# Optimization experiments

Hardware: AMD Instinct MI355X
Metric: run time of the kernel (lower is better)

Reference implementation:

```python
import jax, jax.numpy as jnp
import numpy as np

BN_EPS = 1e-5


def _preconv(x, bn_gamma, bn_beta, bn_mean, bn_var, conv_w, conv_b):
    # nn.Sequential(ReLU, BatchNorm2d(eval mode), Conv2d(in->32, k=1))
    x = jax.nn.relu(x)
    scale = bn_gamma * jax.lax.rsqrt(bn_var + BN_EPS)          # [C]
    x = x * scale[None, :, None, None] + (bn_beta - bn_mean * scale)[None, :, None, None]
    # 1x1 conv == channel matmul
    x = jnp.einsum('bchw,oc->bohw', x, conv_w) + conv_b[None, :, None, None]
    return x


def setup_inputs() -> dict:
    key = jax.random.key(0)
    ks = jax.random.split(key, 8)
    B, Cin, H, W = 8, 80, 160, 320
    return {
        'features_L': jax.random.normal(ks[0], (B, Cin, H, W), dtype=jnp.float32),
        'features_R': jax.random.normal(ks[1], (B, Cin, H, W), dtype=jnp.float32),
        'bn_gamma': jax.random.uniform(ks[2], (Cin,), dtype=jnp.float32, minval=0.5, maxval=1.5),
        'bn_beta': jax.random.normal(ks[3], (Cin,), dtype=jnp.float32) * 0.1,
        'bn_mean': jax.random.normal(ks[4], (Cin,), dtype=jnp.float32) * 0.1,
        'bn_var': jax.random.uniform(ks[5], (Cin,), dtype=jnp.float32, minval=0.5, maxval=1.5),
        'conv_w': jax.random.normal(ks[6], (32, Cin), dtype=jnp.float32) * 0.05,
        'conv_b': jax.random.normal(ks[7], (32,), dtype=jnp.float32) * 0.05,
    }


def reference(features_L, features_R, bn_gamma, bn_beta, bn_mean, bn_var, conv_w, conv_b):
    VOLUME_SIZE = 48  # init kwarg; num_groups = 1 (hardcoded)
    featL = _preconv(features_L, bn_gamma, bn_beta, bn_mean, bn_var, conv_w, conv_b)
    featR = _preconv(features_R, bn_gamma, bn_beta, bn_mean, bn_var, conv_w, conv_b)
    B, C, H, W = featL.shape
    planes = []
    for i in range(VOLUME_SIZE):
        # shift featR right by i with zero padding; zeros in cols < i match the
        # zero-initialized volume entries of the original loop.
        if i > 0:
            shifted = jnp.pad(featR, ((0, 0), (0, 0), (0, 0), (i, 0)))[:, :, :, :W]
        else:
            shifted = featR
        planes.append(jnp.mean(featL * shifted, axis=1))  # [B,H,W]
    volume = jnp.stack(planes, axis=1)  # [B, D, H, W]
    return volume
```

## Files before the change

kernel.cpp:

```cpp
#include <hip/hip_runtime.h>

#define WW   320
#define HH   160
#define CIN  80
#define COUT 32
#define DD   48
#define NB   8
#define VP   84

typedef __bf16 bf16x8 __attribute__((ext_vector_type(8)));
typedef __bf16 bf16x4 __attribute__((ext_vector_type(4)));
typedef float  float4v __attribute__((ext_vector_type(4)));

__global__ __launch_bounds__(320, 2)
void vol_kernel(const float* __restrict__ inL, const float* __restrict__ inR,
                const float* __restrict__ gamma, const float* __restrict__ beta,
                const float* __restrict__ bnmean, const float* __restrict__ bnvar,
                const float* __restrict__ convw, const float* __restrict__ convb,
                float* __restrict__ out)
{
    __shared__ __align__(16) __bf16 fLs[WW * COUT];
    __shared__ __align__(16) __bf16 fRs[WW * COUT];
    __shared__ __align__(16) char   uni[WW * COUT * 2];
    __shared__ __align__(16) float  scs[96];
    __shared__ float  shs[80];
    __shared__ float  biasp[32];
    __shared__ float  scratch[320];

    __bf16* xs2 = (__bf16*)uni;
    float*  vol = (float*)uni;

    const int t = threadIdx.x;
    const int b = blockIdx.x / HH;
    const int h = blockIdx.x % HH;
    const size_t HW = (size_t)HH * WW;
    const int wave = t >> 6, lane = t & 63, ln15 = lane & 15, quad = lane >> 4;
    const int w = t;
    const int sw = (w >> 1) & 3;

    if (t < CIN) {
        float sc = gamma[t] * rsqrtf(bnvar[t] + 1e-5f);
        scs[t] = sc;
        shs[t] = fmaf(-bnmean[t], sc, beta[t]);
    } else if (t < 96) {
        scs[t] = 0.f;
    }
    __syncthreads();

    bf16x8 afr[2][3];
    #pragma unroll
    for (int mt = 0; mt < 2; ++mt) {
        #pragma unroll
        for (int kk = 0; kk < 3; ++kk) {
            const int c0 = kk * 32 + quad * 8;
            bf16x8 a;
            if (c0 < CIN) {
                const float* wp = convw + (mt * 16 + ln15) * CIN + c0;
                float4v w0 = *(const float4v*)wp;
                float4v w1 = *(const float4v*)(wp + 4);
                float4v s0 = *(const float4v*)(scs + c0);
                float4v s1 = *(const float4v*)(scs + c0 + 4);
                #pragma unroll
                for (int j = 0; j < 4; ++j) {
                    a[j]     = (__bf16)(w0[j] * s0[j]);
                    a[j + 4] = (__bf16)(w1[j] * s1[j]);
                }
            } else {
                #pragma unroll
                for (int j = 0; j < 8; ++j) a[j] = (__bf16)0.f;
            }
            afr[mt][kk] = a;
        }
    }
    {
        const int o = t & 31, part = t >> 5;
        float p = 0.f;
        #pragma unroll
        for (int j = 0; j < 8; ++j) {
            int c = part * 8 + j;
            p = fmaf(shs[c], convw[o * CIN + c], p);
        }
        scratch[part * 32 + o] = p;
    }
    __syncthreads();
    if (t < 32) {
        float s = convb[t];
        #pragma unroll
        for (int pt = 0; pt < 10; ++pt) s += scratch[pt * 32 + t];
        biasp[t] = s;
    }

    #pragma unroll 1
    for (int img = 0; img < 2; ++img) {
        const float* __restrict__ px =
            (img ? inR : inL) + ((size_t)b * CIN * HH + h) * WW + w;
        __bf16* f = img ? fRs : fLs;

        float4v acc[2][4];
        #pragma unroll
        for (int mt = 0; mt < 2; ++mt)
            #pragma unroll
            for (int nn = 0; nn < 4; ++nn) acc[mt][nn] = (float4v){0.f, 0.f, 0.f, 0.f};

        float y[32];
        #pragma unroll
        for (int u = 0; u < 32; ++u) y[u] = px[(size_t)u * HW];
        #pragma unroll
        for (int g = 0; g < 4; ++g) {
            bf16x8 pk;
            #pragma unroll
            for (int j = 0; j < 8; ++j) pk[j] = (__bf16)fmaxf(y[g * 8 + j], 0.f);
            *(bf16x8*)(xs2 + w * 32 + ((g ^ sw) << 3)) = pk;
        }
        __syncthreads();

        #pragma unroll
        for (int kk = 0; kk < 3; ++kk) {
            if (kk < 2) {
                #pragma unroll
                for (int u = 0; u < 32; ++u) {
                    int c = (kk + 1) * 32 + u;
                    y[u] = (c < CIN) ? px[(size_t)c * HW] : 0.f;
                }
            }
            #pragma unroll
            for (int nn = 0; nn < 4; ++nn) {
                const int wr = (nn * 5 + wave) * 16 + ln15;
                bf16x8 bv = *(const bf16x8*)(xs2 + wr * 32 +
                                             ((quad ^ ((wr >> 1) & 3)) << 3));
                acc[0][nn] = __builtin_amdgcn_mfma_f32_16x16x32_bf16(afr[0][kk], bv, acc[0][nn], 0, 0, 0);
                acc[1][nn] = __builtin_amdgcn_mfma_f32_16x16x32_bf16(afr[1][kk], bv, acc[1][nn], 0, 0, 0);
            }
            __syncthreads();
            if (kk < 2) {
                #pragma unroll
                for (int g = 0; g < 4; ++g) {
                    bf16x8 pk;
                    #pragma unroll
                    for (int j = 0; j < 8; ++j) pk[j] = (__bf16)fmaxf(y[g * 8 + j], 0.f);
                    *(bf16x8*)(xs2 + w * 32 + ((g ^ sw) << 3)) = pk;
                }
                __syncthreads();
            }
        }

        #pragma unroll
        for (int nn = 0; nn < 4; ++nn) {
            const int wg  = (nn * 5 + wave) * 16 + ln15;
            const int swg = (wg >> 1) & 3;
            #pragma unroll
            for (int mt = 0; mt < 2; ++mt) {
                float4v bi = *(const float4v*)(biasp + mt * 16 + quad * 4);
                bf16x4 o4;
                #pragma unroll
                for (int r = 0; r < 4; ++r)
                    o4[r] = (__bf16)(acc[mt][nn][r] + bi[r]);
                const int g = 2 * mt + (quad >> 1);
                *(bf16x4*)(f + wg * 32 + ((g ^ swg) << 3) + (quad & 1) * 4) = o4;
            }
        }
    }
    __syncthreads();

    for (int pass = 0; pass < 4; ++pass) {
        for (int k = wave; k < 20; k += 5) {
            const int two = k >> 2;
            const int d   = k & 3;
            const int tw  = pass * 5 + two;
            const int tj  = tw - d;
            if (tj >= 0) {
                const int wr = tw * 16 + ln15;
                const int jr = tj * 16 + ln15;
                bf16x8 av = *(const bf16x8*)(fLs + wr * 32 +
                                             ((quad ^ ((wr >> 1) & 3)) << 3));
                bf16x8 bv = *(const bf16x8*)(fRs + jr * 32 +
                                             ((quad ^ ((jr >> 1) & 3)) << 3));
                float4v cz = {0.f, 0.f, 0.f, 0.f};
                float4v dv = __builtin_amdgcn_mfma_f32_16x16x32_bf16(av, bv, cz, 0, 0, 0);
                #pragma unroll
                for (int r = 0; r < 4; ++r) {
                    int row = quad * 4 + r;
                    int i = 16 * d + row - ln15;
                    if (i >= 0 && i < DD)
                        vol[i * VP + two * 16 + row] = dv[r] * (1.f / 32.f);
                }
            }
        }
        __syncthreads();

        for (int s = t; s < DD * 20; s += 320) {
            int i = s / 20, q = s - i * 20;
            int wg0 = pass * 80 + q * 4;
            float4v v = *(const float4v*)(vol + i * VP + q * 4);
            #pragma unroll
            for (int e = 0; e < 4; ++e)
                if (wg0 + e < i) v[e] = 0.f;
            *(float4v*)(out + ((size_t)(b * DD + i) * HH + h) * WW + wg0) = v;
        }
        __syncthreads();
    }
}

extern "C" void kernel_launch(void* const* d_in, const int* in_sizes, int n_in,
                              void* d_out, int out_size, void* d_ws, size_t ws_size,
                              hipStream_t stream) {
    const float* inL    = (const float*)d_in[0];
    const float* inR    = (const float*)d_in[1];
    const float* gamma  = (const float*)d_in[2];
    const float* beta   = (const float*)d_in[3];
    const float* bnmean = (const float*)d_in[4];
    const float* bnvar  = (const float*)d_in[5];
    const float* convw  = (const float*)d_in[6];
    const float* convb  = (const float*)d_in[7];
    float* out = (float*)d_out;

    dim3 grid(NB * HH);
    dim3 block(320);
    vol_kernel<<<grid, block, 0, stream>>>(inL, inR, gamma, beta, bnmean, bnvar,
                                           convw, convb, out);
}
```

Before: 335.2 us.

## Feed conv MFMA directly from registers, shrink LDS, raise occupancy

```diff
diff --git a/kernel.cpp b/kernel.cpp
--- a/kernel.cpp
+++ b/kernel.cpp
@@ -6,13 +6,12 @@
 #define COUT 32
 #define DD   48
 #define NB   8
-#define VP   84
+#define VP2  68
 
 typedef __bf16 bf16x8 __attribute__((ext_vector_type(8)));
-typedef __bf16 bf16x4 __attribute__((ext_vector_type(4)));
 typedef float  float4v __attribute__((ext_vector_type(4)));
 
-__global__ __launch_bounds__(320, 2)
+__global__ __launch_bounds__(320, 4)
 void vol_kernel(const float* __restrict__ inL, const float* __restrict__ inR,
                 const float* __restrict__ gamma, const float* __restrict__ beta,
                 const float* __restrict__ bnmean, const float* __restrict__ bnvar,
@@ -21,22 +20,19 @@
 {
     __shared__ __align__(16) __bf16 fLs[WW * COUT];
     __shared__ __align__(16) __bf16 fRs[WW * COUT];
-    __shared__ __align__(16) char   uni[WW * COUT * 2];
-    __shared__ __align__(16) float  scs[96];
-    __shared__ float  shs[80];
-    __shared__ float  biasp[32];
-    __shared__ float  scratch[320];
-
-    __bf16* xs2 = (__bf16*)uni;
-    float*  vol = (float*)uni;
+    __shared__ __align__(16) float  vol[DD * VP2];
+    __shared__ float biasp[32];
+
+    float* scs     = (float*)fLs;
+    float* shs     = scs + 96;
+    float* scratch = shs + 80;
 
     const int t = threadIdx.x;
     const int b = blockIdx.x / HH;
     const int h = blockIdx.x % HH;
     const size_t HW = (size_t)HH * WW;
     const int wave = t >> 6, lane = t & 63, ln15 = lane & 15, quad = lane >> 4;
-    const int w = t;
-    const int sw = (w >> 1) & 3;
+    const int wb = wave * 64;
 
     if (t < CIN) {
         float sc = gamma[t] * rsqrtf(bnvar[t] + 1e-5f);
@@ -47,15 +43,15 @@
     }
     __syncthreads();
 
-    bf16x8 afr[2][3];
+    bf16x8 bfr[2][3];
     #pragma unroll
-    for (int mt = 0; mt < 2; ++mt) {
+    for (int ot = 0; ot < 2; ++ot) {
         #pragma unroll
         for (int kk = 0; kk < 3; ++kk) {
             const int c0 = kk * 32 + quad * 8;
             bf16x8 a;
             if (c0 < CIN) {
-                const float* wp = convw + (mt * 16 + ln15) * CIN + c0;
+                const float* wp = convw + (ot * 16 + ln15) * CIN + c0;
                 float4v w0 = *(const float4v*)wp;
                 float4v w1 = *(const float4v*)(wp + 4);
                 float4v s0 = *(const float4v*)(scs + c0);
@@ -69,7 +65,7 @@
                 #pragma unroll
                 for (int j = 0; j < 8; ++j) a[j] = (__bf16)0.f;
             }
-            afr[mt][kk] = a;
+            bfr[ot][kk] = a;
         }
     }
     {
@@ -89,84 +85,77 @@
         for (int pt = 0; pt < 10; ++pt) s += scratch[pt * 32 + t];
         biasp[t] = s;
     }
+    __syncthreads();
 
     #pragma unroll 1
     for (int img = 0; img < 2; ++img) {
-        const float* __restrict__ px =
-            (img ? inR : inL) + ((size_t)b * CIN * HH + h) * WW + w;
+        const float* __restrict__ pbase =
+            (img ? inR : inL) + ((size_t)b * CIN * HH + h) * WW;
         __bf16* f = img ? fRs : fLs;
 
-        float4v acc[2][4];
-        #pragma unroll
-        for (int mt = 0; mt < 2; ++mt)
+        const float bi0 = biasp[ln15];
+        const float bi1 = biasp[16 + ln15];
+        float4v acc[4][2];
+        #pragma unroll
+        for (int nt = 0; nt < 4; ++nt) {
+            acc[nt][0] = (float4v){bi0, bi0, bi0, bi0};
+            acc[nt][1] = (float4v){bi1, bi1, bi1, bi1};
+        }
+
+        float y[3][8];
+        auto LOADF = [&](int ft, float (&yy)[8]) {
+            const int nt = ft / 3, kk = ft - nt * 3;
+            if (kk == 2 && quad >= 2) {
+                #pragma unroll
+                for (int j = 0; j < 8; ++j) yy[j] = 0.f;
+            } else {
+                const float* pp = pbase + (size_t)(kk * 32 + quad * 8) * HW
+                                        + (wb + nt * 16 + ln15);
+                #pragma unroll
+                for (int j = 0; j < 8; ++j) yy[j] = pp[(size_t)j * HW];
+            }
+        };
+
+        LOADF(0, y[0]);
+        LOADF(1, y[1]);
+        #pragma unroll
+        for (int ft = 0; ft < 12; ++ft) {
+            if (ft < 10) LOADF(ft + 2, y[(ft + 2) % 3]);
+            const int nt = ft / 3, kk = ft - nt * 3;
+            bf16x8 a;
+            {
+                float (&yy)[8] = y[ft % 3];
+                #pragma unroll
+                for (int j = 0; j < 8; ++j) a[j] = (__bf16)fmaxf(yy[j], 0.f);
+            }
+            acc[nt][0] = __builtin_amdgcn_mfma_f32_16x16x32_bf16(a, bfr[0][kk], acc[nt][0], 0, 0, 0);
+            acc[nt][1] = __builtin_amdgcn_mfma_f32_16x16x32_bf16(a, bfr[1][kk], acc[nt][1], 0, 0, 0);
+        }
+
+        #pragma unroll
+        for (int nt = 0; nt < 4; ++nt) {
+            const int wr0 = wb + nt * 16 + quad * 4;
             #pragma unroll
-            for (int nn = 0; nn < 4; ++nn) acc[mt][nn] = (float4v){0.f, 0.f, 0.f, 0.f};
-
-        float y[32];
-        #pragma unroll
-        for (int u = 0; u < 32; ++u) y[u] = px[(size_t)u * HW];
-        #pragma unroll
-        for (int g = 0; g < 4; ++g) {
-            bf16x8 pk;
-            #pragma unroll
-            for (int j = 0; j < 8; ++j) pk[j] = (__bf16)fmaxf(y[g * 8 + j], 0.f);
-            *(bf16x8*)(xs2 + w * 32 + ((g ^ sw) << 3)) = pk;
-        }
-        __syncthreads();
-
-        #pragma unroll
-        for (int kk = 0; kk < 3; ++kk) {
-            if (kk < 2) {
-                #pragma unroll
-                for (int u = 0; u < 32; ++u) {
-                    int c = (kk + 1) * 32 + u;
-                    y[u] = (c < CIN) ? px[(size_t)c * HW] : 0.f;
+            for (int r = 0; r < 4; ++r) {
+                const int w  = wr0 + r;
+                const int sw = (w >> 1) & 3;
+                #pragma unroll
+                for (int ot = 0; ot < 2; ++ot) {
+                    const int o = ot * 16 + ln15;
+                    f[w * 32 + ((((o >> 3) ^ sw)) << 3) + (o & 7)] =
+                        (__bf16)acc[nt][ot][r];
                 }
             }
-            #pragma unroll
-            for (int nn = 0; nn < 4; ++nn) {
-                const int wr = (nn * 5 + wave) * 16 + ln15;
-                bf16x8 bv = *(const bf16x8*)(xs2 + wr * 32 +
-                                             ((quad ^ ((wr >> 1) & 3)) << 3));
-                acc[0][nn] = __builtin_amdgcn_mfma_f32_16x16x32_bf16(afr[0][kk], bv, acc[0][nn], 0, 0, 0);
-                acc[1][nn] = __builtin_amdgcn_mfma_f32_16x16x32_bf16(afr[1][kk], bv, acc[1][nn], 0, 0, 0);
-            }
-            __syncthreads();
-            if (kk < 2) {
-                #pragma unroll
-                for (int g = 0; g < 4; ++g) {
-                    bf16x8 pk;
-                    #pragma unroll
-                    for (int j = 0; j < 8; ++j) pk[j] = (__bf16)fmaxf(y[g * 8 + j], 0.f);
-                    *(bf16x8*)(xs2 + w * 32 + ((g ^ sw) << 3)) = pk;
-                }
-                __syncthreads();
-            }
-        }
-
-        #pragma unroll
-        for (int nn = 0; nn < 4; ++nn) {
-            const int wg  = (nn * 5 + wave) * 16 + ln15;
-            const int swg = (wg >> 1) & 3;
-            #pragma unroll
-            for (int mt = 0; mt < 2; ++mt) {
-                float4v bi = *(const float4v*)(biasp + mt * 16 + quad * 4);
-                bf16x4 o4;
-                #pragma unroll
-                for (int r = 0; r < 4; ++r)
-                    o4[r] = (__bf16)(acc[mt][nn][r] + bi[r]);
-                const int g = 2 * mt + (quad >> 1);
-                *(bf16x4*)(f + wg * 32 + ((g ^ swg) << 3) + (quad & 1) * 4) = o4;
-            }
-        }
-    }
-    __syncthreads();
-
-    for (int pass = 0; pass < 4; ++pass) {
-        for (int k = wave; k < 20; k += 5) {
+        }
+    }
+    __syncthreads();
+
+    #pragma unroll 1
+    for (int pass = 0; pass < 5; ++pass) {
+        for (int k = wave; k < 16; k += 5) {
             const int two = k >> 2;
             const int d   = k & 3;
-            const int tw  = pass * 5 + two;
+            const int tw  = pass * 4 + two;
             const int tj  = tw - d;
             if (tj >= 0) {
                 const int wr = tw * 16 + ln15;
@@ -182,20 +171,20 @@
                     int row = quad * 4 + r;
                     int i = 16 * d + row - ln15;
                     if (i >= 0 && i < DD)
-                        vol[i * VP + two * 16 + row] = dv[r] * (1.f / 32.f);
+                        vol[i * VP2 + two * 16 + row] = dv[r] * (1.f / 32.f);
                 }
             }
         }
         __syncthreads();
 
-        for (int s = t; s < DD * 20; s += 320) {
-            int i = s / 20, q = s - i * 20;
-            int wg0 = pass * 80 + q * 4;
-            float4v v = *(const float4v*)(vol + i * VP + q * 4);
+        for (int s = t; s < DD * 16; s += 320) {
+            int i = s >> 4, q = s & 15;
+            int w0 = pass * 64 + q * 4;
+            float4v v = *(const float4v*)(vol + i * VP2 + q * 4);
             #pragma unroll
             for (int e = 0; e < 4; ++e)
-                if (wg0 + e < i) v[e] = 0.f;
-            *(float4v*)(out + ((size_t)(b * DD + i) * HH + h) * WW + wg0) = v;
+                if (w0 + e < i) v[e] = 0.f;
+            *(float4v*)(out + ((size_t)(b * DD + i) * HH + h) * WW + w0) = v;
         }
         __syncthreads();
     }
```

Measured after the change: 352.5 us. 5.1% more time.

## Split fused kernel into preconv and volume kernels via bf16 workspace

Applied to the files above, without the earlier changes.

```diff
diff --git a/kernel.cpp b/kernel.cpp
--- a/kernel.cpp
+++ b/kernel.cpp
@@ -7,10 +7,229 @@
 #define DD   48
 #define NB   8
 #define VP   84
+#define VP2  68
 
 typedef __bf16 bf16x8 __attribute__((ext_vector_type(8)));
 typedef __bf16 bf16x4 __attribute__((ext_vector_type(4)));
 typedef float  float4v __attribute__((ext_vector_type(4)));
+
+
+__global__ __launch_bounds__(320, 2)
+void preconv_kernel(const float* __restrict__ inL, const float* __restrict__ inR,
+                    const float* __restrict__ gamma, const float* __restrict__ beta,
+                    const float* __restrict__ bnmean, const float* __restrict__ bnvar,
+                    const float* __restrict__ convw, const float* __restrict__ convb,
+                    __bf16* __restrict__ feat)
+{
+    __shared__ __align__(16) __bf16 xs2[WW * COUT];
+    __shared__ __align__(16) __bf16 fs [WW * COUT];
+    __shared__ __align__(16) float  scs[96];
+    __shared__ float shs[80];
+    __shared__ float biasp[32];
+    __shared__ float scratch[320];
+
+    const int t = threadIdx.x;
+    const int idx = blockIdx.x;
+    const int img = idx / (NB * HH);
+    const int rem = idx - img * (NB * HH);
+    const int b = rem / HH;
+    const int h = rem % HH;
+    const size_t HW = (size_t)HH * WW;
+    const int wave = t >> 6, lane = t & 63, ln15 = lane & 15, quad = lane >> 4;
+    const int w = t;
+    const int sw = (w >> 1) & 3;
+
+    if (t < CIN) {
+        float sc = gamma[t] * rsqrtf(bnvar[t] + 1e-5f);
+        scs[t] = sc;
+        shs[t] = fmaf(-bnmean[t], sc, beta[t]);
+    } else if (t < 96) {
+        scs[t] = 0.f;
+    }
+    __syncthreads();
+
+    bf16x8 afr[2][3];
+    #pragma unroll
+    for (int mt = 0; mt < 2; ++mt) {
+        #pragma unroll
+        for (int kk = 0; kk < 3; ++kk) {
+            const int c0 = kk * 32 + quad * 8;
+            bf16x8 a;
+            if (c0 < CIN) {
+                const float* wp = convw + (mt * 16 + ln15) * CIN + c0;
+                float4v w0 = *(const float4v*)wp;
+                float4v w1 = *(const float4v*)(wp + 4);
+                float4v s0 = *(const float4v*)(scs + c0);
+                float4v s1 = *(const float4v*)(scs + c0 + 4);
+                #pragma unroll
+                for (int j = 0; j < 4; ++j) {
+                    a[j]     = (__bf16)(w0[j] * s0[j]);
+                    a[j + 4] = (__bf16)(w1[j] * s1[j]);
+                }
+            } else {
+                #pragma unroll
+                for (int j = 0; j < 8; ++j) a[j] = (__bf16)0.f;
+            }
+            afr[mt][kk] = a;
+        }
+    }
+    {
+        const int o = t & 31, part = t >> 5;
+        float p = 0.f;
+        #pragma unroll
+        for (int j = 0; j < 8; ++j) {
+            int c = part * 8 + j;
+            p = fmaf(shs[c], convw[o * CIN + c], p);
+        }
+        scratch[part * 32 + o] = p;
+    }
+    __syncthreads();
+    if (t < 32) {
+        float s = convb[t];
+        #pragma unroll
+        for (int pt = 0; pt < 10; ++pt) s += scratch[pt * 32 + t];
+        biasp[t] = s;
+    }
+
+    const float* __restrict__ px =
+        (img ? inR : inL) + ((size_t)b * CIN * HH + h) * WW + w;
+
+    float4v acc[2][4];
+    #pragma unroll
+    for (int mt = 0; mt < 2; ++mt)
+        #pragma unroll
+        for (int nn = 0; nn < 4; ++nn) acc[mt][nn] = (float4v){0.f, 0.f, 0.f, 0.f};
+
+    float y[32];
+    #pragma unroll
+    for (int u = 0; u < 32; ++u) y[u] = px[(size_t)u * HW];
+    #pragma unroll
+    for (int g = 0; g < 4; ++g) {
+        bf16x8 pk;
+        #pragma unroll
+        for (int j = 0; j < 8; ++j) pk[j] = (__bf16)fmaxf(y[g * 8 + j], 0.f);
+        *(bf16x8*)(xs2 + w * 32 + ((g ^ sw) << 3)) = pk;
+    }
+    __syncthreads();
+
+    #pragma unroll
+    for (int kk = 0; kk < 3; ++kk) {
+        if (kk < 2) {
+            #pragma unroll
+            for (int u = 0; u < 32; ++u) {
+                int c = (kk + 1) * 32 + u;
+                y[u] = (c < CIN) ? px[(size_t)c * HW] : 0.f;
+            }
+        }
+        #pragma unroll
+        for (int nn = 0; nn < 4; ++nn) {
+            const int wr = (nn * 5 + wave) * 16 + ln15;
+            bf16x8 bv = *(const bf16x8*)(xs2 + wr * 32 +
+                                         ((quad ^ ((wr >> 1) & 3)) << 3));
+            acc[0][nn] = __builtin_amdgcn_mfma_f32_16x16x32_bf16(afr[0][kk], bv, acc[0][nn], 0, 0, 0);
+            acc[1][nn] = __builtin_amdgcn_mfma_f32_16x16x32_bf16(afr[1][kk], bv, acc[1][nn], 0, 0, 0);
+        }
+        __syncthreads();
+        if (kk < 2) {
+            #pragma unroll
+            for (int g = 0; g < 4; ++g) {
+                bf16x8 pk;
+                #pragma unroll
+                for (int j = 0; j < 8; ++j) pk[j] = (__bf16)fmaxf(y[g * 8 + j], 0.f);
+                *(bf16x8*)(xs2 + w * 32 + ((g ^ sw) << 3)) = pk;
+            }
+            __syncthreads();
+        }
+    }
+
+    #pragma unroll
+    for (int nn = 0; nn < 4; ++nn) {
+        const int wg  = (nn * 5 + wave) * 16 + ln15;
+        const int swg = (wg >> 1) & 3;
+        #pragma unroll
+        for (int mt = 0; mt < 2; ++mt) {
+            float4v bi = *(const float4v*)(biasp + mt * 16 + quad * 4);
+            bf16x4 o4;
+            #pragma unroll
+            for (int r = 0; r < 4; ++r)
+                o4[r] = (__bf16)(acc[mt][nn][r] + bi[r]);
+            const int g = 2 * mt + (quad >> 1);
+            *(bf16x4*)(fs + wg * 32 + ((g ^ swg) << 3) + (quad & 1) * 4) = o4;
+        }
+    }
+    __syncthreads();
+
+    {
+        const float4v* src = (const float4v*)fs;
+        float4v* dst = (float4v*)(feat + (size_t)idx * (WW * COUT));
+        for (int s = t; s < (WW * COUT * 2) / 16; s += 320) dst[s] = src[s];
+    }
+}
+
+__global__ __launch_bounds__(320, 2)
+void volume_kernel(const __bf16* __restrict__ feat, float* __restrict__ out)
+{
+    __shared__ __align__(16) __bf16 fLs[WW * COUT];
+    __shared__ __align__(16) __bf16 fRs[WW * COUT];
+    __shared__ __align__(16) float  vol[DD * VP2];
+
+    const int t = threadIdx.x;
+    const int bh = blockIdx.x;
+    const int b = bh / HH;
+    const int h = bh % HH;
+    const int wave = t >> 6, lane = t & 63, ln15 = lane & 15, quad = lane >> 4;
+
+    {
+        const float4v* srcL = (const float4v*)(feat + (size_t)bh * (WW * COUT));
+        const float4v* srcR = (const float4v*)(feat + (size_t)(NB * HH + bh) * (WW * COUT));
+        float4v* dL = (float4v*)fLs;
+        float4v* dR = (float4v*)fRs;
+        for (int s = t; s < (WW * COUT * 2) / 16; s += 320) {
+            dL[s] = srcL[s];
+            dR[s] = srcR[s];
+        }
+    }
+    __syncthreads();
+
+    #pragma unroll 1
+    for (int pass = 0; pass < 5; ++pass) {
+        for (int k = wave; k < 16; k += 5) {
+            const int two = k >> 2;
+            const int d   = k & 3;
+            const int tw  = pass * 4 + two;
+            const int tj  = tw - d;
+            if (tj >= 0) {
+                const int wr = tw * 16 + ln15;
+                const int jr = tj * 16 + ln15;
+                bf16x8 av = *(const bf16x8*)(fLs + wr * 32 +
+                                             ((quad ^ ((wr >> 1) & 3)) << 3));
+                bf16x8 bv = *(const bf16x8*)(fRs + jr * 32 +
+                                             ((quad ^ ((jr >> 1) & 3)) << 3));
+                float4v cz = {0.f, 0.f, 0.f, 0.f};
+                float4v dv = __builtin_amdgcn_mfma_f32_16x16x32_bf16(av, bv, cz, 0, 0, 0);
+                #pragma unroll
+                for (int r = 0; r < 4; ++r) {
+                    int row = quad * 4 + r;
+                    int i = 16 * d + row - ln15;
+                    if (i >= 0 && i < DD)
+                        vol[i * VP2 + two * 16 + row] = dv[r] * (1.f / 32.f);
+                }
+            }
+        }
+        __syncthreads();
+
+        for (int s = t; s < DD * 16; s += 320) {
+            int i = s >> 4, q = s & 15;
+            int w0 = pass * 64 + q * 4;
+            float4v v = *(const float4v*)(vol + i * VP2 + q * 4);
+            #pragma unroll
+            for (int e = 0; e < 4; ++e)
+                if (w0 + e < i) v[e] = 0.f;
+            *(float4v*)(out + ((size_t)(b * DD + i) * HH + h) * WW + w0) = v;
+        }
+        __syncthreads();
+    }
+}
 
 __global__ __launch_bounds__(320, 2)
 void vol_kernel(const float* __restrict__ inL, const float* __restrict__ inR,
@@ -214,8 +433,15 @@
     const float* convb  = (const float*)d_in[7];
     float* out = (float*)d_out;
 
-    dim3 grid(NB * HH);
-    dim3 block(320);
-    vol_kernel<<<grid, block, 0, stream>>>(inL, inR, gamma, beta, bnmean, bnvar,
-                                           convw, convb, out);
+    const size_t need = (size_t)2 * NB * HH * WW * COUT * sizeof(__bf16);
+
+    if (d_ws != nullptr && ws_size >= need) {
+        __bf16* feat = (__bf16*)d_ws;
+        preconv_kernel<<<dim3(2 * NB * HH), dim3(320), 0, stream>>>(
+            inL, inR, gamma, beta, bnmean, bnvar, convw, convb, feat);
+        volume_kernel<<<dim3(NB * HH), dim3(320), 0, stream>>>(feat, out);
+    } else {
+        vol_kernel<<<dim3(NB * HH), dim3(320), 0, stream>>>(
+            inL, inR, gamma, beta, bnmean, bnvar, convw, convb, out);
+    }
 }
```

New measurement: 341.4 us. No clear change (+1.8%).
